# Optimization experiments

Hardware: AMD Instinct MI355X
Metric: run time of the kernel (lower is better)

Reference implementation:

```python
import jax, jax.numpy as jnp
import numpy as np

B, S, D, H = 4, 2048, 1024, 16
HD = D // H


def setup_inputs() -> dict:
    key = jax.random.key(0)
    ks = jax.random.split(key, 12)
    def lin(k):
        return jax.random.normal(k, (D, D), dtype=jnp.float32) * 0.02
    return {
        "query": jax.random.normal(ks[0], (B, S, D), dtype=jnp.float32),
        "key": jax.random.normal(ks[1], (B, S, D), dtype=jnp.float32),
        "value": jax.random.normal(ks[2], (B, S, D), dtype=jnp.float32),
        "Wq": lin(ks[3]), "bq": jnp.zeros((D,), jnp.float32),
        "Wk": lin(ks[4]), "bk": jnp.zeros((D,), jnp.float32),
        "Wv": lin(ks[5]), "bv": jnp.zeros((D,), jnp.float32),
        "Wo": lin(ks[6]), "bo": jnp.zeros((D,), jnp.float32),
        "pad_mask": jnp.ones((B, S), dtype=jnp.int32),
    }


def reference(query, key, value, Wq, bq, Wk, bk, Wv, bv, Wo, bo, pad_mask):
    # torch nn.Linear convention: y = x @ W.T + b
    Q = query @ Wq.T + bq   # [B,Sq,D]
    K = key @ Wk.T + bk     # [B,Sk,D]
    V = value @ Wv.T + bv
    Sq, Sk = Q.shape[1], K.shape[1]
    Q = Q.reshape(B, Sq, H, HD).transpose(0, 2, 1, 3)  # [B,H,Sq,hd]
    K = K.reshape(B, Sk, H, HD).transpose(0, 2, 1, 3)
    V = V.reshape(B, Sk, H, HD).transpose(0, 2, 1, 3)
    scores = jnp.einsum('bhqd,bhkd->bhqk', Q, K) / jnp.sqrt(jnp.float32(HD))
    # causal (lookahead) mask
    causal = jnp.tril(jnp.ones((Sq, Sk), dtype=bool))
    scores = jnp.where(causal[None, None], scores, -jnp.inf)
    # pad mask broadcast [B,1,Sq,1]
    pm = (pad_mask[:, None, :, None] != 0)
    scores = jnp.where(pm, scores, -jnp.inf)
    attn = jax.nn.softmax(scores, axis=-1)
    out = jnp.einsum('bhqk,bhkd->bhqd', attn, V)  # [B,H,Sq,hd]
    out = out.transpose(0, 2, 1, 3).reshape(B, Sq, D)
    return out @ Wo.T + bo
```

## Files before the change

kernel.cpp:

```cpp
#include <hip/hip_runtime.h>
#include <hip/hip_bf16.h>
#include <stdint.h>

typedef __attribute__((ext_vector_type(8))) short bf16x8;
typedef __attribute__((ext_vector_type(4))) float f32x4;

#define HD 64
#define NH 16
#define SEQ 2048
#define DM 1024

#define GLDS16(gp, lp)                                                      \
    __builtin_amdgcn_global_load_lds(                                       \
        (const __attribute__((address_space(1))) void*)(gp),                \
        (__attribute__((address_space(3))) void*)(lp), 16, 0, 0)

__device__ inline bf16x8 cvt8(const float* __restrict__ p) {
    float4 a = *(const float4*)p;
    float4 b = *(const float4*)(p + 4);
    union { bf16x8 v; __hip_bfloat16 e[8]; } u;
    u.e[0] = __float2bfloat16(a.x); u.e[1] = __float2bfloat16(a.y);
    u.e[2] = __float2bfloat16(a.z); u.e[3] = __float2bfloat16(a.w);
    u.e[4] = __float2bfloat16(b.x); u.e[5] = __float2bfloat16(b.y);
    u.e[6] = __float2bfloat16(b.z); u.e[7] = __float2bfloat16(b.w);
    return u.v;
}

__global__ __launch_bounds__(256)
void cvtw(const float* __restrict__ a, const float* __restrict__ b,
          const float* __restrict__ c, const float* __restrict__ d,
          __hip_bfloat16* __restrict__ o)
{
    int g = blockIdx.x * 256 + threadIdx.x;
    int t = g * 4;
    const float* src;
    switch (t >> 20) {
        case 0: src = a; break;
        case 1: src = b; break;
        case 2: src = c; break;
        default: src = d; break;
    }
    float4 v = *(const float4*)(src + (t & 0xFFFFF));
    union { ushort4 u; __hip_bfloat16 e[4]; } w;
    w.e[0] = __float2bfloat16(v.x); w.e[1] = __float2bfloat16(v.y);
    w.e[2] = __float2bfloat16(v.z); w.e[3] = __float2bfloat16(v.w);
    *(ushort4*)(o + t) = w.u;
}

__global__ __launch_bounds__(256)
void cvtx(const float* __restrict__ src, __hip_bfloat16* __restrict__ dst)
{
    int t = (blockIdx.x * 256 + threadIdx.x) * 8;
    *(bf16x8*)(dst + t) = cvt8(src + t);
}

template<int OMODE>
__global__ __launch_bounds__(256)
void gemm16(const __hip_bfloat16* __restrict__ X,
            const __hip_bfloat16* __restrict__ Wb,
            const float* __restrict__ bias,
            void* __restrict__ Yv,
            int M, int N, int K)
{
    __shared__ alignas(16) __hip_bfloat16 As[128 * 32];
    __shared__ alignas(16) __hip_bfloat16 Bs[128 * 32];

    const int tid  = threadIdx.x;
    const int lane = tid & 63;
    const int wv   = tid >> 6;
    const int quad = lane >> 4;
    const int l15  = lane & 15;
    const int wm   = (wv >> 1) * 64;
    const int wn   = (wv & 1) * 64;
    const int m0   = blockIdx.y * 128;
    const int n0   = blockIdx.x * 128;

    f32x4 acc[4][4] = {};

    for (int k0 = 0; k0 < K; k0 += 32) {
        #pragma unroll
        for (int it = 0; it < 2; ++it) {
            int c = tid + it * 256;
            int row = c >> 2, cg = c & 3;
            GLDS16(&X[(size_t)(m0 + row) * K + k0 + cg * 8],
                   (char*)As + (size_t)c * 16);
            GLDS16(&Wb[(size_t)(n0 + row) * K + k0 + cg * 8],
                   (char*)Bs + (size_t)c * 16);
        }
        __syncthreads();

        bf16x8 af[4], bfr[4];
        #pragma unroll
        for (int i = 0; i < 4; ++i)
            af[i] = *(const bf16x8*)(&As[(wm + i * 16 + l15) * 32 + quad * 8]);
        #pragma unroll
        for (int j = 0; j < 4; ++j)
            bfr[j] = *(const bf16x8*)(&Bs[(wn + j * 16 + l15) * 32 + quad * 8]);

        #pragma unroll
        for (int i = 0; i < 4; ++i)
            #pragma unroll
            for (int j = 0; j < 4; ++j)
                acc[i][j] = __builtin_amdgcn_mfma_f32_16x16x32_bf16(
                    af[i], bfr[j], acc[i][j], 0, 0, 0);
        __syncthreads();
    }

    #pragma unroll
    for (int j = 0; j < 4; ++j) {
        int n = n0 + wn + j * 16 + l15;
        float bv = bias[n];
        int h = n >> 6, hd = n & 63;
        #pragma unroll
        for (int i = 0; i < 4; ++i) {
            int mb = m0 + wm + i * 16 + quad * 4;
            if (OMODE == 0) {
                __hip_bfloat16* Y = (__hip_bfloat16*)Yv;
                #pragma unroll
                for (int r = 0; r < 4; ++r) {
                    int m = mb + r;
                    int b = m >> 11, s = m & 2047;
                    Y[((size_t)(b * NH + h) * SEQ + s) * HD + hd] =
                        __float2bfloat16(acc[i][j][r] + bv);
                }
            } else if (OMODE == 2) {
                __hip_bfloat16* Y = (__hip_bfloat16*)Yv;
                int b = mb >> 11, s = mb & 2047;
                union { ushort4 u; __hip_bfloat16 e[4]; } w;
                #pragma unroll
                for (int r = 0; r < 4; ++r)
                    w.e[r] = __float2bfloat16(acc[i][j][r] + bv);
                *(ushort4*)(&Y[((size_t)(b * NH + h) * HD + hd) * SEQ + s]) = w.u;
            } else {
                float* Y = (float*)Yv;
                #pragma unroll
                for (int r = 0; r < 4; ++r)
                    Y[(size_t)(mb + r) * N + n] = acc[i][j][r] + bv;
            }
        }
    }
}

__global__ __launch_bounds__(256)
void attn(const __hip_bfloat16* __restrict__ Qh,
          const __hip_bfloat16* __restrict__ Kh,
          const __hip_bfloat16* __restrict__ Vt,
          __hip_bfloat16* __restrict__ O)
{
    __shared__ alignas(16) __hip_bfloat16 Ks[64 * 64];
    __shared__ alignas(16) __hip_bfloat16 VsT[80 * 64];
    __shared__ alignas(16) __hip_bfloat16 Ps[4][32 * 64];

    const int tid  = threadIdx.x;
    const int lane = tid & 63;
    const int wv   = tid >> 6;
    const int quad = lane >> 4;
    const int l15  = lane & 15;
    const int bh   = blockIdx.y;
    const int b    = bh >> 4;
    const int h    = bh & 15;
    const int p    = blockIdx.x;
    const int sa   = p;
    const int sb   = 31 - p;
    const int sw   = l15 & 7;

    const __hip_bfloat16* Qp  = Qh + (size_t)bh * SEQ * HD;
    const __hip_bfloat16* Kp  = Kh + (size_t)bh * SEQ * HD;
    const __hip_bfloat16* Vtp = Vt + (size_t)bh * HD * SEQ;

    {
        int idx = 64 * 64 + tid * 4;
        __hip_bfloat16 v = __float2bfloat16(tid < 16 ? 1.0f : 0.0f);
        union { ushort4 u; __hip_bfloat16 e[4]; } w;
        w.e[0] = v; w.e[1] = v; w.e[2] = v; w.e[3] = v;
        *(ushort4*)(&VsT[idx]) = w.u;
    }

    bf16x8 aq[2][2];
    #pragma unroll
    for (int s = 0; s < 2; ++s) {
        int qb = (s ? sb : sa) * 64;
        #pragma unroll
        for (int ks = 0; ks < 2; ++ks)
            aq[s][ks] = *(const bf16x8*)(
                &Qp[(size_t)(qb + wv * 16 + l15) * HD + ks * 32 + quad * 8]);
    }

    f32x4 o[2][4] = {};
    f32x4 o5[2]   = {};
    const float SC = 0.18033688f;

    const int ntiles = 32 - p;
    for (int t = 0; t < ntiles; ++t) {
        const int kv0 = t * 64;
        const bool s0act = (t <= sa);
        __syncthreads();
        #pragma unroll
        for (int it = 0; it < 2; ++it) {
            int c = tid + it * 256;
            int row = c >> 3, cg = (c & 7) ^ (row & 7);
            GLDS16(&Kp[(size_t)(kv0 + row) * HD + cg * 8],
                   (char*)Ks + (size_t)c * 16);
            GLDS16(&Vtp[(size_t)row * SEQ + kv0 + cg * 8],
                   (char*)VsT + (size_t)c * 16);
        }
        __syncthreads();

        #pragma unroll
        for (int jk = 0; jk < 4; ++jk) {
            f32x4 s0 = {}, s1 = {};
            #pragma unroll
            for (int ks = 0; ks < 2; ++ks) {
                bf16x8 kf = *(const bf16x8*)(
                    &Ks[(jk * 16 + l15) * 64 + (((ks * 4 + quad) ^ sw) * 8)]);
                if (s0act)
                    s0 = __builtin_amdgcn_mfma_f32_16x16x32_bf16(aq[0][ks], kf, s0, 0, 0, 0);
                s1 = __builtin_amdgcn_mfma_f32_16x16x32_bf16(aq[1][ks], kf, s1, 0, 0, 0);
            }
            int kv = kv0 + jk * 16 + l15;
            int colsw = ((jk * 2 + (l15 >> 3)) * 8);
            int cl = l15 & 7;
            #pragma unroll
            for (int s = 0; s < 2; ++s) {
                if (s == 0 && !s0act) continue;
                f32x4 sv = (s == 0) ? s0 : s1;
                int rl0 = s * 16 + quad * 4;
                int strip = s ? sb : sa;
                bool needmask = (t == strip);
                #pragma unroll
                for (int r = 0; r < 4; ++r) {
                    float e = __builtin_amdgcn_exp2f(fminf(sv[r] * SC, 30.f));
                    if (needmask) {
                        int q = strip * 64 + wv * 16 + quad * 4 + r;
                        e = (kv <= q) ? e : 0.f;
                    }
                    int rl = rl0 + r;
                    Ps[wv][rl * 64 + (colsw ^ ((rl & 7) * 8)) + cl] = __float2bfloat16(e);
                }
            }
        }

        bf16x8 pa[2][2];
        #pragma unroll
        for (int s = 0; s < 2; ++s) {
            if (s == 0 && !s0act) continue;
            #pragma unroll
            for (int ks = 0; ks < 2; ++ks)
                pa[s][ks] = *(const bf16x8*)(
                    &Ps[wv][(s * 16 + l15) * 64 + (((ks * 4 + quad) ^ sw) * 8)]);
        }
        #pragma unroll
        for (int jn = 0; jn < 4; ++jn) {
            #pragma unroll
            for (int ks = 0; ks < 2; ++ks) {
                bf16x8 vb = *(const bf16x8*)(
                    &VsT[(jn * 16 + l15) * 64 + (((ks * 4 + quad) ^ sw) * 8)]);
                if (s0act)
                    o[0][jn] = __builtin_amdgcn_mfma_f32_16x16x32_bf16(pa[0][ks], vb, o[0][jn], 0, 0, 0);
                o[1][jn] = __builtin_amdgcn_mfma_f32_16x16x32_bf16(pa[1][ks], vb, o[1][jn], 0, 0, 0);
            }
        }
        #pragma unroll
        for (int ks = 0; ks < 2; ++ks) {
            bf16x8 vb = *(const bf16x8*)(
                &VsT[(64 + l15) * 64 + (((ks * 4 + quad) ^ sw) * 8)]);
            if (s0act)
                o5[0] = __builtin_amdgcn_mfma_f32_16x16x32_bf16(pa[0][ks], vb, o5[0], 0, 0, 0);
            o5[1] = __builtin_amdgcn_mfma_f32_16x16x32_bf16(pa[1][ks], vb, o5[1], 0, 0, 0);
        }
    }

    #pragma unroll
    for (int s = 0; s < 2; ++s) {
        float inv[4];
        #pragma unroll
        for (int r = 0; r < 4; ++r)
            inv[r] = 1.0f / __shfl(o5[s][r], lane & 48, 64);
        int strip = s ? sb : sa;
        #pragma unroll
        for (int jn = 0; jn < 4; ++jn) {
            #pragma unroll
            for (int r = 0; r < 4; ++r) {
                int q = strip * 64 + wv * 16 + quad * 4 + r;
                O[((size_t)(b * SEQ + q)) * DM + h * HD + jn * 16 + l15] =
                    __float2bfloat16(o[s][jn][r] * inv[r]);
            }
        }
    }
}

extern "C" void kernel_launch(void* const* d_in, const int* in_sizes, int n_in,
                              void* d_out, int out_size, void* d_ws, size_t ws_size,
                              hipStream_t stream)
{
    const float* query = (const float*)d_in[0];
    const float* key_  = (const float*)d_in[1];
    const float* value = (const float*)d_in[2];
    const float* Wq = (const float*)d_in[3];
    const float* bq = (const float*)d_in[4];
    const float* Wk = (const float*)d_in[5];
    const float* bk = (const float*)d_in[6];
    const float* Wv = (const float*)d_in[7];
    const float* bv = (const float*)d_in[8];
    const float* Wo = (const float*)d_in[9];
    const float* bo = (const float*)d_in[10];

    const size_t WSZ = (size_t)1024 * 1024;
    const size_t MAT = (size_t)8192 * 1024;
    __hip_bfloat16* wb = (__hip_bfloat16*)d_ws;
    __hip_bfloat16* Qh = wb + 4 * WSZ;
    __hip_bfloat16* Kh = Qh + MAT;
    __hip_bfloat16* Vt = Kh + MAT;
    __hip_bfloat16* Oa = Vt + MAT;
    float* out = (float*)d_out;

    dim3 bb(256);
    dim3 gg(8, 64);
    cvtw<<<4096, bb, 0, stream>>>(Wq, Wk, Wv, Wo, wb);
    cvtx<<<4096, bb, 0, stream>>>(query, Oa);
    gemm16<0><<<gg, bb, 0, stream>>>(Oa, wb,           bq, Qh, 8192, 1024, 1024);
    cvtx<<<4096, bb, 0, stream>>>(key_, Oa);
    gemm16<0><<<gg, bb, 0, stream>>>(Oa, wb + WSZ,     bk, Kh, 8192, 1024, 1024);
    cvtx<<<4096, bb, 0, stream>>>(value, Oa);
    gemm16<2><<<gg, bb, 0, stream>>>(Oa, wb + 2 * WSZ, bv, Vt, 8192, 1024, 1024);
    attn<<<dim3(16, 64), bb, 0, stream>>>(Qh, Kh, Vt, Oa);
    gemm16<1><<<gg, bb, 0, stream>>>(Oa, wb + 3 * WSZ, bo, out, 8192, 1024, 1024);
}
```

Before: 414.4 us.

## Double-buffer K/V tiles and serialize strips; compute row sums via shuffles

The attention loop now walks the two query strips one after the other instead of sharing each K/V tile between both strips. K/V tiles are double-buffered in LDS, so the next tile's global-to-LDS load is issued before the current tile is computed, and one barrier per iteration is dropped. The softmax denominator no longer comes from an extra ones-row MFMA over V. It is accumulated in registers and reduced with lane shuffles. The cost is that shared K/V tiles are now loaded twice (for strips A and B), which roughly doubles K/V loads per block.

```diff
diff --git a/kernel.cpp b/kernel.cpp
--- a/kernel.cpp
+++ b/kernel.cpp
@@ -141,15 +141,60 @@
     }
 }
 
+__device__ __forceinline__ void attn_tile(
+    const bf16x8 (&aqs)[2], f32x4 (&os)[4], float (&lis)[4],
+    const __hip_bfloat16* __restrict__ K_, const __hip_bfloat16* __restrict__ V_,
+    __hip_bfloat16* __restrict__ Pw,
+    int kv0, int qrow0, bool diag, int quad, int l15, int sw)
+{
+    const float SC = 0.18033688f;
+    #pragma unroll
+    for (int jk = 0; jk < 4; ++jk) {
+        f32x4 sv = {};
+        #pragma unroll
+        for (int ks = 0; ks < 2; ++ks) {
+            bf16x8 kf = *(const bf16x8*)(
+                &K_[(jk * 16 + l15) * 64 + (((ks * 4 + quad) ^ sw) * 8)]);
+            sv = __builtin_amdgcn_mfma_f32_16x16x32_bf16(aqs[ks], kf, sv, 0, 0, 0);
+        }
+        int kv = kv0 + jk * 16 + l15;
+        int colsw = ((jk * 2 + (l15 >> 3)) * 8);
+        int cl = l15 & 7;
+        #pragma unroll
+        for (int r = 0; r < 4; ++r) {
+            float e = __builtin_amdgcn_exp2f(fminf(sv[r] * SC, 30.f));
+            if (diag) {
+                int q = qrow0 + quad * 4 + r;
+                e = (kv <= q) ? e : 0.f;
+            }
+            lis[r] += e;
+            int rl = quad * 4 + r;
+            Pw[rl * 64 + (colsw ^ ((rl & 7) * 8)) + cl] = __float2bfloat16(e);
+        }
+    }
+    bf16x8 pa[2];
+    #pragma unroll
+    for (int ks = 0; ks < 2; ++ks)
+        pa[ks] = *(const bf16x8*)(&Pw[l15 * 64 + (((ks * 4 + quad) ^ sw) * 8)]);
+    #pragma unroll
+    for (int jn = 0; jn < 4; ++jn)
+        #pragma unroll
+        for (int ks = 0; ks < 2; ++ks) {
+            bf16x8 vb = *(const bf16x8*)(
+                &V_[(jn * 16 + l15) * 64 + (((ks * 4 + quad) ^ sw) * 8)]);
+            os[jn] = __builtin_amdgcn_mfma_f32_16x16x32_bf16(pa[ks], vb, os[jn], 0, 0, 0);
+        }
+}
+
 __global__ __launch_bounds__(256)
 void attn(const __hip_bfloat16* __restrict__ Qh,
           const __hip_bfloat16* __restrict__ Kh,
           const __hip_bfloat16* __restrict__ Vt,
           __hip_bfloat16* __restrict__ O)
 {
-    __shared__ alignas(16) __hip_bfloat16 Ks[64 * 64];
-    __shared__ alignas(16) __hip_bfloat16 VsT[80 * 64];
-    __shared__ alignas(16) __hip_bfloat16 Ps[4][32 * 64];
+    __shared__ alignas(16) __hip_bfloat16 Ks[2][64 * 64];
+    __shared__ alignas(16) __hip_bfloat16 VsT[2][64 * 64];
+    __shared__ alignas(16) __hip_bfloat16 Ps[4][16 * 64];
 
     const int tid  = threadIdx.x;
     const int lane = tid & 63;
@@ -168,14 +213,6 @@
     const __hip_bfloat16* Kp  = Kh + (size_t)bh * SEQ * HD;
     const __hip_bfloat16* Vtp = Vt + (size_t)bh * HD * SEQ;
 
-    {
-        int idx = 64 * 64 + tid * 4;
-        __hip_bfloat16 v = __float2bfloat16(tid < 16 ? 1.0f : 0.0f);
-        union { ushort4 u; __hip_bfloat16 e[4]; } w;
-        w.e[0] = v; w.e[1] = v; w.e[2] = v; w.e[3] = v;
-        *(ushort4*)(&VsT[idx]) = w.u;
-    }
-
     bf16x8 aq[2][2];
     #pragma unroll
     for (int s = 0; s < 2; ++s) {
@@ -186,97 +223,66 @@
                 &Qp[(size_t)(qb + wv * 16 + l15) * HD + ks * 32 + quad * 8]);
     }
 
-    f32x4 o[2][4] = {};
-    f32x4 o5[2]   = {};
-    const float SC = 0.18033688f;
-
-    const int ntiles = 32 - p;
-    for (int t = 0; t < ntiles; ++t) {
-        const int kv0 = t * 64;
-        const bool s0act = (t <= sa);
-        __syncthreads();
+    f32x4 o[2][4]  = {};
+    float li[2][4] = {};
+
+    __hip_bfloat16* Pw = Ps[wv];
+
+    auto STAGE = [&](int bufi, int kv0) {
         #pragma unroll
         for (int it = 0; it < 2; ++it) {
             int c = tid + it * 256;
             int row = c >> 3, cg = (c & 7) ^ (row & 7);
             GLDS16(&Kp[(size_t)(kv0 + row) * HD + cg * 8],
-                   (char*)Ks + (size_t)c * 16);
+                   (char*)Ks[bufi] + (size_t)c * 16);
             GLDS16(&Vtp[(size_t)row * SEQ + kv0 + cg * 8],
-                   (char*)VsT + (size_t)c * 16);
-        }
+                   (char*)VsT[bufi] + (size_t)c * 16);
+        }
+    };
+
+    const int nit = sa + sb + 2;
+
+    STAGE(0, 0);
+
+    for (int i = 0; i < nit; ++i) {
         __syncthreads();
 
-        #pragma unroll
-        for (int jk = 0; jk < 4; ++jk) {
-            f32x4 s0 = {}, s1 = {};
-            #pragma unroll
-            for (int ks = 0; ks < 2; ++ks) {
-                bf16x8 kf = *(const bf16x8*)(
-                    &Ks[(jk * 16 + l15) * 64 + (((ks * 4 + quad) ^ sw) * 8)]);
-                if (s0act)
-                    s0 = __builtin_amdgcn_mfma_f32_16x16x32_bf16(aq[0][ks], kf, s0, 0, 0, 0);
-                s1 = __builtin_amdgcn_mfma_f32_16x16x32_bf16(aq[1][ks], kf, s1, 0, 0, 0);
-            }
-            int kv = kv0 + jk * 16 + l15;
-            int colsw = ((jk * 2 + (l15 >> 3)) * 8);
-            int cl = l15 & 7;
-            #pragma unroll
-            for (int s = 0; s < 2; ++s) {
-                if (s == 0 && !s0act) continue;
-                f32x4 sv = (s == 0) ? s0 : s1;
-                int rl0 = s * 16 + quad * 4;
-                int strip = s ? sb : sa;
-                bool needmask = (t == strip);
-                #pragma unroll
-                for (int r = 0; r < 4; ++r) {
-                    float e = __builtin_amdgcn_exp2f(fminf(sv[r] * SC, 30.f));
-                    if (needmask) {
-                        int q = strip * 64 + wv * 16 + quad * 4 + r;
-                        e = (kv <= q) ? e : 0.f;
-                    }
-                    int rl = rl0 + r;
-                    Ps[wv][rl * 64 + (colsw ^ ((rl & 7) * 8)) + cl] = __float2bfloat16(e);
-                }
-            }
-        }
-
-        bf16x8 pa[2][2];
-        #pragma unroll
-        for (int s = 0; s < 2; ++s) {
-            if (s == 0 && !s0act) continue;
-            #pragma unroll
-            for (int ks = 0; ks < 2; ++ks)
-                pa[s][ks] = *(const bf16x8*)(
-                    &Ps[wv][(s * 16 + l15) * 64 + (((ks * 4 + quad) ^ sw) * 8)]);
-        }
-        #pragma unroll
-        for (int jn = 0; jn < 4; ++jn) {
-            #pragma unroll
-            for (int ks = 0; ks < 2; ++ks) {
-                bf16x8 vb = *(const bf16x8*)(
-                    &VsT[(jn * 16 + l15) * 64 + (((ks * 4 + quad) ^ sw) * 8)]);
-                if (s0act)
-                    o[0][jn] = __builtin_amdgcn_mfma_f32_16x16x32_bf16(pa[0][ks], vb, o[0][jn], 0, 0, 0);
-                o[1][jn] = __builtin_amdgcn_mfma_f32_16x16x32_bf16(pa[1][ks], vb, o[1][jn], 0, 0, 0);
-            }
-        }
-        #pragma unroll
-        for (int ks = 0; ks < 2; ++ks) {
-            bf16x8 vb = *(const bf16x8*)(
-                &VsT[(64 + l15) * 64 + (((ks * 4 + quad) ^ sw) * 8)]);
-            if (s0act)
-                o5[0] = __builtin_amdgcn_mfma_f32_16x16x32_bf16(pa[0][ks], vb, o5[0], 0, 0, 0);
-            o5[1] = __builtin_amdgcn_mfma_f32_16x16x32_bf16(pa[1][ks], vb, o5[1], 0, 0, 0);
-        }
+        int ni = i + 1;
+        if (ni < nit) {
+            int t2 = (ni <= sb) ? ni : ni - sb - 1;
+            STAGE(ni & 1, t2 * 64);
+        }
+
+        const int cb    = i & 1;
+        const bool isB  = (i <= sb);
+        const int t     = isB ? i : i - sb - 1;
+        const int strip = isB ? sb : sa;
+        const int kv0   = t * 64;
+        const bool diag = (t == strip);
+        const int qrow0 = strip * 64 + wv * 16;
+
+        const __hip_bfloat16* K_ = Ks[cb];
+        const __hip_bfloat16* V_ = VsT[cb];
+
+        if (isB)
+            attn_tile(aq[1], o[1], li[1], K_, V_, Pw, kv0, qrow0, diag, quad, l15, sw);
+        else
+            attn_tile(aq[0], o[0], li[0], K_, V_, Pw, kv0, qrow0, diag, quad, l15, sw);
     }
 
     #pragma unroll
     for (int s = 0; s < 2; ++s) {
+        int strip = s ? sb : sa;
         float inv[4];
         #pragma unroll
-        for (int r = 0; r < 4; ++r)
-            inv[r] = 1.0f / __shfl(o5[s][r], lane & 48, 64);
-        int strip = s ? sb : sa;
+        for (int r = 0; r < 4; ++r) {
+            float v = li[s][r];
+            v += __shfl_xor(v, 1);
+            v += __shfl_xor(v, 2);
+            v += __shfl_xor(v, 4);
+            v += __shfl_xor(v, 8);
+            inv[r] = 1.0f / v;
+        }
         #pragma unroll
         for (int jn = 0; jn < 4; ++jn) {
             #pragma unroll
```

Measured after the change: 389.0 us. 6.1% less time.
